# Kernel optimization log

Hardware: AMD Instinct MI355X
Metric: run time of the kernel (lower is better)

Reference implementation:

```python
import jax, jax.numpy as jnp
import numpy as np

B, NI, NH = 1024, 32, 1024  # batch, num_inputs, num_hidden


def _masks(ni, nh):
    # get_mask semantics from the torch source (mask shape = (out_features, in_features))
    in_deg_input = jnp.arange(ni) % ni                # mask_type='input'
    hid_deg = jnp.arange(nh) % (ni - 1)               # hidden degrees
    out_deg_output = jnp.arange(2 * ni) % ni - 1      # mask_type='output'
    m1 = (hid_deg[:, None] >= in_deg_input[None, :]).astype(jnp.float32)   # (NH, NI)
    m2 = (hid_deg[:, None] >= hid_deg[None, :]).astype(jnp.float32)        # (NH, NH)
    m3 = (out_deg_output[:, None] >= hid_deg[None, :]).astype(jnp.float32) # (2*NI, NH)
    return m1, m2, m3


def setup_inputs() -> dict:
    key = jax.random.key(0)
    ks = jax.random.split(key, 7)
    s1 = 1.0 / np.sqrt(NI)
    s2 = 1.0 / np.sqrt(NH)
    return {
        "inputs": jax.random.normal(ks[0], (B, NI), dtype=jnp.float32),
        "W1": jax.random.normal(ks[1], (NH, NI), dtype=jnp.float32) * s1,
        "b1": jax.random.normal(ks[2], (NH,), dtype=jnp.float32) * s1,
        "W2": jax.random.normal(ks[3], (NH, NH), dtype=jnp.float32) * s2,
        "b2": jax.random.normal(ks[4], (NH,), dtype=jnp.float32) * s2,
        "W3": jax.random.normal(ks[5], (2 * NI, NH), dtype=jnp.float32) * s2,
        "b3": jax.random.normal(ks[6], (2 * NI,), dtype=jnp.float32) * s2,
    }


def reference(inputs, W1, b1, W2, b2, W3, b3):
    ni = inputs.shape[1]
    nh = W1.shape[0]
    m1, m2, m3 = _masks(ni, nh)
    M1, M2, M3 = W1 * m1, W2 * m2, W3 * m3  # masked weights, precomputed once

    def net(x):  # 3-layer masked MLP -> (B, 2*ni) params
        h = jax.nn.relu(x @ M1.T + b1)
        h = jax.nn.relu(h @ M2.T + b2)
        return h @ M3.T + b3

    def step(x, i):
        p = net(x)                       # (B, 2*ni)
        m_i = p[:, i]                    # mean for dim i
        a_i = jnp.tanh(p[:, ni + i])     # log-scale for dim i (use_tanh=True)
        x_i = inputs[:, i] * jnp.exp(a_i) + m_i
        return x.at[:, i].set(x_i), -a_i

    x, neg_a = jax.lax.scan(step, jnp.zeros_like(inputs), jnp.arange(ni))
    J = neg_a.sum(axis=0)[:, None]       # (B, 1)
    return x, J
```

## Files before the change

kernel.cpp:

```cpp
#include <hip/hip_runtime.h>
#include <hip/hip_fp16.h>
#include <math.h>

#define NI   32
#define NH   1024
#define NB   1024

#define OFF_B1S 0
#define OFF_B2S 1056
#define OFF_W3S 2080
#define OFF_W1B 67616
#define OFF_PB  84512

__device__ __forceinline__ int base_of(int d) { return (d == 0) ? 0 : 33 * d + 1; }

__device__ __forceinline__ unsigned short f2h(float f) {
    return __half_as_ushort(__float2half(f));
}

typedef _Float16 h2v __attribute__((ext_vector_type(2)));
__device__ __forceinline__ h2v as_h2(unsigned u) {
    union { unsigned u; h2v h; } c; c.u = u; return c.h;
}
__device__ __forceinline__ float fdot2u(unsigned a, unsigned b, float c) {
#if __has_builtin(__builtin_amdgcn_fdot2)
    return __builtin_amdgcn_fdot2(as_h2(a), as_h2(b), c, false);
#else
    h2v ah = as_h2(a), bh = as_h2(b);
    return fmaf((float)ah.x, (float)bh.x, fmaf((float)ah.y, (float)bh.y, c));
#endif
}

template <int CTRL>
__device__ __forceinline__ float dpp_add(float s) {
    int t = __builtin_amdgcn_update_dpp(0, __float_as_int(s), CTRL, 0xF, 0xF, true);
    return s + __int_as_float(t);
}

__device__ __forceinline__ float wave_allsum(float s) {
    s = dpp_add<0xB1>(s);
    s = dpp_add<0x4E>(s);
    s = dpp_add<0x141>(s);
    s = dpp_add<0x140>(s);
#if __has_builtin(__builtin_amdgcn_permlane16_swap)
    {
        using uint2v = __attribute__((ext_vector_type(2))) unsigned int;
        uint2v r = __builtin_amdgcn_permlane16_swap(
            __float_as_uint(s), __float_as_uint(s), false, false);
        s = __uint_as_float(r.x) + __uint_as_float(r.y);
    }
#else
    s += __int_as_float(__builtin_amdgcn_ds_swizzle(__float_as_int(s), 0x401F));
#endif
#if __has_builtin(__builtin_amdgcn_permlane32_swap)
    {
        using uint2v = __attribute__((ext_vector_type(2))) unsigned int;
        uint2v r = __builtin_amdgcn_permlane32_swap(
            __float_as_uint(s), __float_as_uint(s), false, false);
        s = __uint_as_float(r.x) + __uint_as_float(r.y);
    }
#else
    s += __shfl_xor(s, 32, 64);
#endif
    return s;
}

template <int CNT>
__device__ __forceinline__ void prep_w2_cls(int d, int oh0, const float* __restrict__ W2,
                                            unsigned short* __restrict__ pb16, int t,
                                            float (*tile)[65]) {
    const int bse = base_of(d);
#pragma unroll 1
    for (int e = t; e < CNT * 64; e += 256) {
        int k = e >> 6, c = e & 63;
        int og = d + 31 * k;
        tile[k][c] = W2[(size_t)og * NH + oh0 + c];
    }
    __syncthreads();
#pragma unroll 1
    for (int e = t; e < 64 * CNT; e += 256) {
        int oh_l = e / CNT;
        int k = e - oh_l * CNT;
        int oh = oh0 + oh_l;
        int dd = oh % 31, u = oh / 31;
        int sg = bse + k;
        float v = (d >= dd) ? tile[k][oh_l] : 0.0f;
        size_t a = (size_t)((dd * 17 + (u >> 1)) * 256 + (sg >> 2)) * 8
                 + (sg & 3) * 2 + (u & 1);
        pb16[a] = f2h(v);
    }
}

__global__ __launch_bounds__(256) void prep_all(const float* __restrict__ W1,
        const float* __restrict__ b1, const float* __restrict__ W2,
        const float* __restrict__ b2, const float* __restrict__ W3,
        float* __restrict__ ws) {
    __shared__ float tile[34][65];
    const int bid = blockIdx.x, t = threadIdx.x;
    unsigned short* pb16 = (unsigned short*)(ws + OFF_PB);
    if (bid < 496) {
        int d = bid >> 4, oh0 = (bid & 15) * 64;
        if (d == 0) prep_w2_cls<34>(0, oh0, W2, pb16, t, tile);
        else        prep_w2_cls<33>(d, oh0, W2, pb16, t, tile);
    } else if (bid < 560) {
        const int o  = bid - 496;
        const int od = (o & 31) - 1;
#pragma unroll 1
        for (int e = t; e < NH; e += 256) {
            int dd = e % 31;
            int k  = e / 31;
            int su = (dd == 0) ? k : 33 * dd + 1 + k;
            float v = (od >= dd) ? W3[(size_t)o * NH + e] : 0.0f;
            ws[OFF_W3S + (size_t)o * NH + su] = v;
        }
    } else {
        const int og = (bid - 560) * 256 + t;
        const int dd = og % 31;
        const int k  = og / 31;
        const int su = (dd == 0) ? k : 33 * dd + 1 + k;
        ws[OFF_B1S + su] = b1[og];
        ws[OFF_B2S + su] = b2[og];
        unsigned* w1b32 = (unsigned*)(ws + OFF_W1B);
        const float4* wrow = (const float4*)(W1 + (size_t)og * NI);
        float4 r[8];
#pragma unroll
        for (int q4 = 0; q4 < 8; ++q4) r[q4] = wrow[q4];
        const float* rf = (const float*)&r[0];
#pragma unroll
        for (int jp = 0; jp < 16; ++jp) {
            float v0 = (dd >= 2 * jp)     ? rf[2 * jp]     : 0.0f;
            float v1 = (dd >= 2 * jp + 1) ? rf[2 * jp + 1] : 0.0f;
            unsigned pk = (unsigned)f2h(v0) | ((unsigned)f2h(v1) << 16);
            w1b32[(size_t)jp * 1056 + su] = pk;
        }
    }
}

__device__ __forceinline__ void consume_pair(uint4 g, uint2 av,
                                             float4& acc0, float4& acc1) {
    acc0.x = fdot2u(av.x, g.x, acc0.x);
    acc0.y = fdot2u(av.x, g.y, acc0.y);
    acc0.z = fdot2u(av.x, g.z, acc0.z);
    acc0.w = fdot2u(av.x, g.w, acc0.w);
    acc1.x = fdot2u(av.y, g.x, acc1.x);
    acc1.y = fdot2u(av.y, g.y, acc1.y);
    acc1.z = fdot2u(av.y, g.z, acc1.z);
    acc1.w = fdot2u(av.y, g.w, acc1.w);
}

__global__ __launch_bounds__(256, 2) void made_scan(
        const float* __restrict__ inputs,
        const float* __restrict__ b3,
        const float* __restrict__ ws,
        float* __restrict__ out) {
    __shared__ float    xsS[4][2][36];
    __shared__ unsigned xsH[4][2][20];
    __shared__ unsigned a1H[4][36];
    __shared__ float part[2][4][4];
    __shared__ float b3S[64];
    __shared__ float xinS[2][NI];

    const int lane = threadIdx.x & 63;
    const int w    = threadIdx.x >> 6;
    const int pairity = ((blockIdx.x >> 8) ^ blockIdx.x) & 1;
    const int q    = w ^ (pairity * 3);
    const int gb   = q * 256;
    const int row0 = blockIdx.x * 2;

    const float* b1s = ws + OFF_B1S;
    const float* b2s = ws + OFF_B2S;
    const float* W3s = ws + OFF_W3S;
    const unsigned* W1B = (const unsigned*)(ws + OFF_W1B);
    const uint4*    PB  = (const uint4*)(ws + OFF_PB);

    float4 acc0 = ((const float4*)(b2s + gb))[lane];
    float4 acc1 = acc0;
    float J0 = 0.f, J1 = 0.f;

    if (w == 0) {
        b3S[lane] = b3[lane];
        if (lane < NI) {
            xinS[0][lane] = inputs[row0 * NI + lane];
            xinS[1][lane] = inputs[(row0 + 1) * NI + lane];
        }
    }
    {
        float* px = &xsS[w][0][0];
        for (int k = lane; k < 72; k += 64) px[k] = 0.f;
        unsigned* ph = &xsH[w][0][0];
        for (int k = lane; k < 40; k += 64) ph[k] = 0u;
    }
    __syncthreads();

    {
        float p00 = b3S[0], p01 = b3S[NI];
        float e20 = __expf(2.f * fminf(p01, 15.f));
        float ta  = (e20 - 1.f) / (e20 + 1.f);
        float es  = __expf(ta);
        float x0  = fmaf(xinS[0][0], es, p00);
        float x1  = fmaf(xinS[1][0], es, p00);
        J0 -= ta; J1 -= ta;
        if (lane == 0) {
            xsS[w][0][0] = x0; xsS[w][1][0] = x1;
            ((unsigned short*)&xsH[w][0][0])[0] = f2h(x0);
            ((unsigned short*)&xsH[w][1][0])[0] = f2h(x1);
        }
    }

#pragma unroll 1
    for (int i = 1; i < NI; ++i) {
        const int dd   = i - 1;
        const int goff = base_of(dd);
        const int cnt  = (i == 1) ? 34 : 33;
        const bool doB = (gb + 256 > goff);
        const bool doC = (gb < 33 * i + 1);

        float4 wa = make_float4(0, 0, 0, 0), wb = make_float4(0, 0, 0, 0);
        if (doC) {
            wa = ((const float4*)(W3s + (size_t)i * NH + gb))[lane];
            wb = ((const float4*)(W3s + (size_t)(NI + i) * NH + gb))[lane];
        }

        if (doB) {
            const uint4* pbase = PB + (size_t)(dd * 17) * 256 + (gb >> 2) + lane;
            uint4 G1[9];
#pragma unroll
            for (int u2 = 0; u2 < 9; ++u2) G1[u2] = pbase[u2 * 256];
            __builtin_amdgcn_sched_barrier(0);

            const int su = goff + lane;
            float bz = b1s[su];
            unsigned wk[16];
#pragma unroll
            for (int k = 0; k < 16; ++k) wk[k] = W1B[k * 1056 + su];
            float zA0 = bz, zA1 = 0, zA2 = 0, zA3 = 0;
            float zB0 = bz, zB1 = 0, zB2 = 0, zB3 = 0;
#pragma unroll
            for (int q4 = 0; q4 < 4; ++q4) {
                uint4 xp0 = *(const uint4*)&xsH[w][0][4 * q4];
                uint4 xp1 = *(const uint4*)&xsH[w][1][4 * q4];
                zA0 = fdot2u(xp0.x, wk[4 * q4 + 0], zA0);
                zB0 = fdot2u(xp1.x, wk[4 * q4 + 0], zB0);
                zA1 = fdot2u(xp0.y, wk[4 * q4 + 1], zA1);
                zB1 = fdot2u(xp1.y, wk[4 * q4 + 1], zB1);
                zA2 = fdot2u(xp0.z, wk[4 * q4 + 2], zA2);
                zB2 = fdot2u(xp1.z, wk[4 * q4 + 2], zB2);
                zA3 = fdot2u(xp0.w, wk[4 * q4 + 3], zA3);
                zB3 = fdot2u(xp1.w, wk[4 * q4 + 3], zB3);
            }
            const bool ok = lane < cnt;
            float a0 = ok ? fmaxf((zA0 + zA1) + (zA2 + zA3), 0.f) : 0.f;
            float a1 = ok ? fmaxf((zB0 + zB1) + (zB2 + zB3), 0.f) : 0.f;
            if (lane < 36) {
                unsigned short* ah = (unsigned short*)&a1H[w][0];
                int u2 = lane >> 1, h = lane & 1;
                ah[u2 * 4 + h]     = f2h(a0);
                ah[u2 * 4 + 2 + h] = f2h(a1);
            }
            __builtin_amdgcn_sched_barrier(0);

            uint4 G2[8];
#pragma unroll
            for (int u2 = 0; u2 < 8; ++u2) G2[u2] = pbase[(9 + u2) * 256];
            __builtin_amdgcn_sched_barrier(0);
#pragma unroll
            for (int u2 = 0; u2 < 9; ++u2)
                consume_pair(G1[u2], *(const uint2*)&a1H[w][2 * u2], acc0, acc1);
            __builtin_amdgcn_sched_barrier(0);
#pragma unroll
            for (int u2 = 0; u2 < 8; ++u2)
                consume_pair(G2[u2], *(const uint2*)&a1H[w][18 + 2 * u2], acc0, acc1);
        }

        float s00 = 0, s01 = 0, s10 = 0, s11 = 0;
        if (doC) {
            float hx, hy, hz, hw;
            hx = fmaxf(acc0.x, 0.f); hy = fmaxf(acc0.y, 0.f);
            hz = fmaxf(acc0.z, 0.f); hw = fmaxf(acc0.w, 0.f);
            s00 = fmaf(wa.x, hx, fmaf(wa.y, hy, fmaf(wa.z, hz, wa.w * hw)));
            s01 = fmaf(wb.x, hx, fmaf(wb.y, hy, fmaf(wb.z, hz, wb.w * hw)));
            hx = fmaxf(acc1.x, 0.f); hy = fmaxf(acc1.y, 0.f);
            hz = fmaxf(acc1.z, 0.f); hw = fmaxf(acc1.w, 0.f);
            s10 = fmaf(wa.x, hx, fmaf(wa.y, hy, fmaf(wa.z, hz, wa.w * hw)));
            s11 = fmaf(wb.x, hx, fmaf(wb.y, hy, fmaf(wb.z, hz, wb.w * hw)));
            s00 = wave_allsum(s00); s01 = wave_allsum(s01);
            s10 = wave_allsum(s10); s11 = wave_allsum(s11);
        }
        if (lane == 0)
            *((float4*)&part[i & 1][w][0]) = make_float4(s00, s01, s10, s11);
        __syncthreads();

        const float* pb = &part[i & 1][0][0];
        float4 q0 = ((const float4*)pb)[0], q1 = ((const float4*)pb)[1];
        float4 q2 = ((const float4*)pb)[2], q3 = ((const float4*)pb)[3];
        float bi  = b3S[i];
        float bia = b3S[NI + i];
        float p00 = ((q0.x + q1.x) + (q2.x + q3.x)) + bi;
        float p01 = ((q0.y + q1.y) + (q2.y + q3.y)) + bia;
        float p10 = ((q0.z + q1.z) + (q2.z + q3.z)) + bi;
        float p11 = ((q0.w + q1.w) + (q2.w + q3.w)) + bia;
        float e20 = __expf(2.f * fminf(p01, 15.f));
        float ta0 = (e20 - 1.f) / (e20 + 1.f);
        float x0  = fmaf(xinS[0][i], __expf(ta0), p00);
        float e21 = __expf(2.f * fminf(p11, 15.f));
        float ta1 = (e21 - 1.f) / (e21 + 1.f);
        float x1  = fmaf(xinS[1][i], __expf(ta1), p10);
        J0 -= ta0; J1 -= ta1;
        if (lane == 0) {
            xsS[w][0][i] = x0; xsS[w][1][i] = x1;
            ((unsigned short*)&xsH[w][0][0])[i] = f2h(x0);
            ((unsigned short*)&xsH[w][1][0])[i] = f2h(x1);
        }
    }

    if (w == 0) {
        if (lane < NI) {
            out[row0 * NI + lane]       = xsS[0][0][lane];
            out[(row0 + 1) * NI + lane] = xsS[0][1][lane];
        }
        if (lane == 0) {
            out[NB * NI + row0]     = J0;
            out[NB * NI + row0 + 1] = J1;
        }
    }
}

extern "C" void kernel_launch(void* const* d_in, const int* in_sizes, int n_in,
                              void* d_out, int out_size, void* d_ws, size_t ws_size,
                              hipStream_t stream) {
    const float* inputs = (const float*)d_in[0];
    const float* W1     = (const float*)d_in[1];
    const float* b1     = (const float*)d_in[2];
    const float* W2     = (const float*)d_in[3];
    const float* b2     = (const float*)d_in[4];
    const float* W3     = (const float*)d_in[5];
    const float* b3     = (const float*)d_in[6];
    float* out = (float*)d_out;
    float* ws  = (float*)d_ws;

    prep_all<<<564, 256, 0, stream>>>(W1, b1, W2, b2, W3, ws);
    made_scan<<<NB / 2, 256, 0, stream>>>(inputs, b3, ws, out);
}
```

Before: 140.4 us.

## Prefetch next step's layer-2 weights across barrier and skip zero W1 groups

Hoists the first nine packed W2 tile loads out of the loop and prefetches the next iteration's G1 slice during the current step. The global-memory latency then overlaps the barrier and the serial tail math. The layer-1 dot product now only processes input groups that can be nonzero for step i, skipping masked W1 reads. The __syncthreads is replaced by an LDS-only waitcnt plus s_barrier, so outstanding global prefetches are not drained at the barrier. This raises register pressure from holding G1 across iterations.

```diff
diff --git a/kernel.cpp b/kernel.cpp
--- a/kernel.cpp
+++ b/kernel.cpp
@@ -207,6 +207,14 @@
         }
     }
 
+    uint4 G1[9];
+    {
+        const uint4* pb0 = PB + (gb >> 2) + lane;
+#pragma unroll
+        for (int u2 = 0; u2 < 9; ++u2) G1[u2] = pb0[u2 * 256];
+    }
+    __builtin_amdgcn_sched_barrier(0);
+
 #pragma unroll 1
     for (int i = 1; i < NI; ++i) {
         const int dd   = i - 1;
@@ -222,32 +230,27 @@
         }
 
         if (doB) {
-            const uint4* pbase = PB + (size_t)(dd * 17) * 256 + (gb >> 2) + lane;
-            uint4 G1[9];
-#pragma unroll
-            for (int u2 = 0; u2 < 9; ++u2) G1[u2] = pbase[u2 * 256];
-            __builtin_amdgcn_sched_barrier(0);
-
             const int su = goff + lane;
             float bz = b1s[su];
-            unsigned wk[16];
-#pragma unroll
-            for (int k = 0; k < 16; ++k) wk[k] = W1B[k * 1056 + su];
+            const int kmax2 = (i + 1) >> 1;
             float zA0 = bz, zA1 = 0, zA2 = 0, zA3 = 0;
             float zB0 = bz, zB1 = 0, zB2 = 0, zB3 = 0;
-#pragma unroll
-            for (int q4 = 0; q4 < 4; ++q4) {
+            auto pa_group = [&](int q4) {
                 uint4 xp0 = *(const uint4*)&xsH[w][0][4 * q4];
                 uint4 xp1 = *(const uint4*)&xsH[w][1][4 * q4];
-                zA0 = fdot2u(xp0.x, wk[4 * q4 + 0], zA0);
-                zB0 = fdot2u(xp1.x, wk[4 * q4 + 0], zB0);
-                zA1 = fdot2u(xp0.y, wk[4 * q4 + 1], zA1);
-                zB1 = fdot2u(xp1.y, wk[4 * q4 + 1], zB1);
-                zA2 = fdot2u(xp0.z, wk[4 * q4 + 2], zA2);
-                zB2 = fdot2u(xp1.z, wk[4 * q4 + 2], zB2);
-                zA3 = fdot2u(xp0.w, wk[4 * q4 + 3], zA3);
-                zB3 = fdot2u(xp1.w, wk[4 * q4 + 3], zB3);
-            }
+                unsigned wk0 = W1B[(4 * q4 + 0) * 1056 + su];
+                unsigned wk1 = W1B[(4 * q4 + 1) * 1056 + su];
+                unsigned wk2 = W1B[(4 * q4 + 2) * 1056 + su];
+                unsigned wk3 = W1B[(4 * q4 + 3) * 1056 + su];
+                zA0 = fdot2u(xp0.x, wk0, zA0); zB0 = fdot2u(xp1.x, wk0, zB0);
+                zA1 = fdot2u(xp0.y, wk1, zA1); zB1 = fdot2u(xp1.y, wk1, zB1);
+                zA2 = fdot2u(xp0.z, wk2, zA2); zB2 = fdot2u(xp1.z, wk2, zB2);
+                zA3 = fdot2u(xp0.w, wk3, zA3); zB3 = fdot2u(xp1.w, wk3, zB3);
+            };
+            pa_group(0);
+            if (kmax2 > 4)  pa_group(1);
+            if (kmax2 > 8)  pa_group(2);
+            if (kmax2 > 12) pa_group(3);
             const bool ok = lane < cnt;
             float a0 = ok ? fmaxf((zA0 + zA1) + (zA2 + zA3), 0.f) : 0.f;
             float a1 = ok ? fmaxf((zB0 + zB1) + (zB2 + zB3), 0.f) : 0.f;
@@ -261,11 +264,20 @@
 
             uint4 G2[8];
 #pragma unroll
-            for (int u2 = 0; u2 < 8; ++u2) G2[u2] = pbase[(9 + u2) * 256];
+            for (int u2 = 0; u2 < 8; ++u2) {
+                const uint4* pbase = PB + (size_t)(dd * 17) * 256 + (gb >> 2) + lane;
+                G2[u2] = pbase[(9 + u2) * 256];
+            }
             __builtin_amdgcn_sched_barrier(0);
 #pragma unroll
             for (int u2 = 0; u2 < 9; ++u2)
                 consume_pair(G1[u2], *(const uint2*)&a1H[w][2 * u2], acc0, acc1);
+
+            if (gb + 256 > 33 * i + 1) {
+                const uint4* pbn = PB + (size_t)(i * 17) * 256 + (gb >> 2) + lane;
+#pragma unroll
+                for (int u2 = 0; u2 < 9; ++u2) G1[u2] = pbn[u2 * 256];
+            }
             __builtin_amdgcn_sched_barrier(0);
 #pragma unroll
             for (int u2 = 0; u2 < 8; ++u2)
@@ -288,7 +300,11 @@
         }
         if (lane == 0)
             *((float4*)&part[i & 1][w][0]) = make_float4(s00, s01, s10, s11);
-        __syncthreads();
+
+        __builtin_amdgcn_sched_barrier(0);
+        asm volatile("s_waitcnt lgkmcnt(0)" ::: "memory");
+        __builtin_amdgcn_s_barrier();
+        __builtin_amdgcn_sched_barrier(0);
 
         const float* pb = &part[i & 1][0][0];
         float4 q0 = ((const float4*)pb)[0], q1 = ((const float4*)pb)[1];
```

Result: slower. 151.4 us (+7.8%).

## Process four batch rows per block to reuse streamed W2 weights

Applied to the files above, without the earlier changes.

Each block now handles four batch rows instead of two. Every W2/W1/W3 weight fragment loaded from global memory is reused across four rows' accumulators, which halves weight traffic per row. The grid shrinks from 512 to 256 blocks and launch bounds drop to one block per SM. The per-block parity swizzle of wave-to-column assignment is removed. The cost is more registers per thread, and the grid may be too small to fill all CUs on MI355X (256 CUs), which reduces parallelism and latency hiding.

```diff
diff --git a/kernel.cpp b/kernel.cpp
--- a/kernel.cpp
+++ b/kernel.cpp
@@ -136,36 +136,34 @@
     }
 }
 
-__device__ __forceinline__ void consume_pair(uint4 g, uint2 av,
-                                             float4& acc0, float4& acc1) {
-    acc0.x = fdot2u(av.x, g.x, acc0.x);
-    acc0.y = fdot2u(av.x, g.y, acc0.y);
-    acc0.z = fdot2u(av.x, g.z, acc0.z);
-    acc0.w = fdot2u(av.x, g.w, acc0.w);
-    acc1.x = fdot2u(av.y, g.x, acc1.x);
-    acc1.y = fdot2u(av.y, g.y, acc1.y);
-    acc1.z = fdot2u(av.y, g.z, acc1.z);
-    acc1.w = fdot2u(av.y, g.w, acc1.w);
-}
-
-__global__ __launch_bounds__(256, 2) void made_scan(
+__device__ __forceinline__ void consume_pair4(uint4 g, uint4 av,
+        float4& c0, float4& c1, float4& c2, float4& c3) {
+    c0.x = fdot2u(av.x, g.x, c0.x); c0.y = fdot2u(av.x, g.y, c0.y);
+    c0.z = fdot2u(av.x, g.z, c0.z); c0.w = fdot2u(av.x, g.w, c0.w);
+    c1.x = fdot2u(av.y, g.x, c1.x); c1.y = fdot2u(av.y, g.y, c1.y);
+    c1.z = fdot2u(av.y, g.z, c1.z); c1.w = fdot2u(av.y, g.w, c1.w);
+    c2.x = fdot2u(av.z, g.x, c2.x); c2.y = fdot2u(av.z, g.y, c2.y);
+    c2.z = fdot2u(av.z, g.z, c2.z); c2.w = fdot2u(av.z, g.w, c2.w);
+    c3.x = fdot2u(av.w, g.x, c3.x); c3.y = fdot2u(av.w, g.y, c3.y);
+    c3.z = fdot2u(av.w, g.z, c3.z); c3.w = fdot2u(av.w, g.w, c3.w);
+}
+
+__global__ __launch_bounds__(256, 1) void made_scan(
         const float* __restrict__ inputs,
         const float* __restrict__ b3,
         const float* __restrict__ ws,
         float* __restrict__ out) {
-    __shared__ float    xsS[4][2][36];
-    __shared__ unsigned xsH[4][2][20];
-    __shared__ unsigned a1H[4][36];
-    __shared__ float part[2][4][4];
-    __shared__ float b3S[64];
-    __shared__ float xinS[2][NI];
+    __shared__ float    xsS[4][4][36];
+    __shared__ unsigned xsH[4][4][20];
+    __shared__ uint4    a1H4[4][18];
+    __shared__ float    part[2][4][8];
+    __shared__ float    b3S[64];
+    __shared__ float    xinS[4][NI];
 
     const int lane = threadIdx.x & 63;
     const int w    = threadIdx.x >> 6;
-    const int pairity = ((blockIdx.x >> 8) ^ blockIdx.x) & 1;
-    const int q    = w ^ (pairity * 3);
-    const int gb   = q * 256;
-    const int row0 = blockIdx.x * 2;
+    const int gb   = w * 256;
+    const int row0 = blockIdx.x * 4;
 
     const float* b1s = ws + OFF_B1S;
     const float* b2s = ws + OFF_B2S;
@@ -173,22 +171,23 @@
     const unsigned* W1B = (const unsigned*)(ws + OFF_W1B);
     const uint4*    PB  = (const uint4*)(ws + OFF_PB);
 
-    float4 acc0 = ((const float4*)(b2s + gb))[lane];
-    float4 acc1 = acc0;
-    float J0 = 0.f, J1 = 0.f;
+    float4 bcc = ((const float4*)(b2s + gb))[lane];
+    float4 acc0 = bcc, acc1 = bcc, acc2 = bcc, acc3 = bcc;
+    float J0 = 0.f, J1 = 0.f, J2 = 0.f, J3 = 0.f;
 
     if (w == 0) {
         b3S[lane] = b3[lane];
         if (lane < NI) {
-            xinS[0][lane] = inputs[row0 * NI + lane];
-            xinS[1][lane] = inputs[(row0 + 1) * NI + lane];
+#pragma unroll
+            for (int r = 0; r < 4; ++r)
+                xinS[r][lane] = inputs[(row0 + r) * NI + lane];
         }
     }
     {
         float* px = &xsS[w][0][0];
-        for (int k = lane; k < 72; k += 64) px[k] = 0.f;
+        for (int k = lane; k < 144; k += 64) px[k] = 0.f;
         unsigned* ph = &xsH[w][0][0];
-        for (int k = lane; k < 40; k += 64) ph[k] = 0u;
+        for (int k = lane; k < 80; k += 64) ph[k] = 0u;
     }
     __syncthreads();
 
@@ -197,13 +196,18 @@
         float e20 = __expf(2.f * fminf(p01, 15.f));
         float ta  = (e20 - 1.f) / (e20 + 1.f);
         float es  = __expf(ta);
-        float x0  = fmaf(xinS[0][0], es, p00);
-        float x1  = fmaf(xinS[1][0], es, p00);
-        J0 -= ta; J1 -= ta;
+        float x0 = fmaf(xinS[0][0], es, p00);
+        float x1 = fmaf(xinS[1][0], es, p00);
+        float x2 = fmaf(xinS[2][0], es, p00);
+        float x3 = fmaf(xinS[3][0], es, p00);
+        J0 -= ta; J1 -= ta; J2 -= ta; J3 -= ta;
         if (lane == 0) {
             xsS[w][0][0] = x0; xsS[w][1][0] = x1;
+            xsS[w][2][0] = x2; xsS[w][3][0] = x3;
             ((unsigned short*)&xsH[w][0][0])[0] = f2h(x0);
             ((unsigned short*)&xsH[w][1][0])[0] = f2h(x1);
+            ((unsigned short*)&xsH[w][2][0])[0] = f2h(x2);
+            ((unsigned short*)&xsH[w][3][0])[0] = f2h(x3);
         }
     }
 
@@ -233,94 +237,138 @@
             unsigned wk[16];
 #pragma unroll
             for (int k = 0; k < 16; ++k) wk[k] = W1B[k * 1056 + su];
-            float zA0 = bz, zA1 = 0, zA2 = 0, zA3 = 0;
-            float zB0 = bz, zB1 = 0, zB2 = 0, zB3 = 0;
+            float z[4][4];
+#pragma unroll
+            for (int r = 0; r < 4; ++r) {
+                z[r][0] = bz; z[r][1] = 0.f; z[r][2] = 0.f; z[r][3] = 0.f;
+            }
 #pragma unroll
             for (int q4 = 0; q4 < 4; ++q4) {
                 uint4 xp0 = *(const uint4*)&xsH[w][0][4 * q4];
                 uint4 xp1 = *(const uint4*)&xsH[w][1][4 * q4];
-                zA0 = fdot2u(xp0.x, wk[4 * q4 + 0], zA0);
-                zB0 = fdot2u(xp1.x, wk[4 * q4 + 0], zB0);
-                zA1 = fdot2u(xp0.y, wk[4 * q4 + 1], zA1);
-                zB1 = fdot2u(xp1.y, wk[4 * q4 + 1], zB1);
-                zA2 = fdot2u(xp0.z, wk[4 * q4 + 2], zA2);
-                zB2 = fdot2u(xp1.z, wk[4 * q4 + 2], zB2);
-                zA3 = fdot2u(xp0.w, wk[4 * q4 + 3], zA3);
-                zB3 = fdot2u(xp1.w, wk[4 * q4 + 3], zB3);
+                uint4 xp2 = *(const uint4*)&xsH[w][2][4 * q4];
+                uint4 xp3 = *(const uint4*)&xsH[w][3][4 * q4];
+                unsigned k0 = wk[4 * q4 + 0], k1 = wk[4 * q4 + 1];
+                unsigned k2 = wk[4 * q4 + 2], k3 = wk[4 * q4 + 3];
+                z[0][0] = fdot2u(xp0.x, k0, z[0][0]);
+                z[0][1] = fdot2u(xp0.y, k1, z[0][1]);
+                z[0][2] = fdot2u(xp0.z, k2, z[0][2]);
+                z[0][3] = fdot2u(xp0.w, k3, z[0][3]);
+                z[1][0] = fdot2u(xp1.x, k0, z[1][0]);
+                z[1][1] = fdot2u(xp1.y, k1, z[1][1]);
+                z[1][2] = fdot2u(xp1.z, k2, z[1][2]);
+                z[1][3] = fdot2u(xp1.w, k3, z[1][3]);
+                z[2][0] = fdot2u(xp2.x, k0, z[2][0]);
+                z[2][1] = fdot2u(xp2.y, k1, z[2][1]);
+                z[2][2] = fdot2u(xp2.z, k2, z[2][2]);
+                z[2][3] = fdot2u(xp2.w, k3, z[2][3]);
+                z[3][0] = fdot2u(xp3.x, k0, z[3][0]);
+                z[3][1] = fdot2u(xp3.y, k1, z[3][1]);
+                z[3][2] = fdot2u(xp3.z, k2, z[3][2]);
+                z[3][3] = fdot2u(xp3.w, k3, z[3][3]);
             }
             const bool ok = lane < cnt;
-            float a0 = ok ? fmaxf((zA0 + zA1) + (zA2 + zA3), 0.f) : 0.f;
-            float a1 = ok ? fmaxf((zB0 + zB1) + (zB2 + zB3), 0.f) : 0.f;
+            float a0 = ok ? fmaxf((z[0][0] + z[0][1]) + (z[0][2] + z[0][3]), 0.f) : 0.f;
+            float a1 = ok ? fmaxf((z[1][0] + z[1][1]) + (z[1][2] + z[1][3]), 0.f) : 0.f;
+            float a2 = ok ? fmaxf((z[2][0] + z[2][1]) + (z[2][2] + z[2][3]), 0.f) : 0.f;
+            float a3 = ok ? fmaxf((z[3][0] + z[3][1]) + (z[3][2] + z[3][3]), 0.f) : 0.f;
             if (lane < 36) {
-                unsigned short* ah = (unsigned short*)&a1H[w][0];
+                unsigned short* ah = (unsigned short*)&a1H4[w][0];
                 int u2 = lane >> 1, h = lane & 1;
-                ah[u2 * 4 + h]     = f2h(a0);
-                ah[u2 * 4 + 2 + h] = f2h(a1);
+                ah[u2 * 8 + 0 + h] = f2h(a0);
+                ah[u2 * 8 + 2 + h] = f2h(a1);
+                ah[u2 * 8 + 4 + h] = f2h(a2);
+                ah[u2 * 8 + 6 + h] = f2h(a3);
             }
             __builtin_amdgcn_sched_barrier(0);
 
             uint4 G2[8];
-#pragma unroll
-            for (int u2 = 0; u2 < 8; ++u2) G2[u2] = pbase[(9 + u2) * 256];
+            {
+#pragma unroll
+                for (int u2 = 0; u2 < 8; ++u2) G2[u2] = pbase[(9 + u2) * 256];
+            }
             __builtin_amdgcn_sched_barrier(0);
 #pragma unroll
             for (int u2 = 0; u2 < 9; ++u2)
-                consume_pair(G1[u2], *(const uint2*)&a1H[w][2 * u2], acc0, acc1);
+                consume_pair4(G1[u2], a1H4[w][u2], acc0, acc1, acc2, acc3);
             __builtin_amdgcn_sched_barrier(0);
 #pragma unroll
             for (int u2 = 0; u2 < 8; ++u2)
-                consume_pair(G2[u2], *(const uint2*)&a1H[w][18 + 2 * u2], acc0, acc1);
-        }
-
-        float s00 = 0, s01 = 0, s10 = 0, s11 = 0;
+                consume_pair4(G2[u2], a1H4[w][9 + u2], acc0, acc1, acc2, acc3);
+        }
+
+        float s0[4] = {0, 0, 0, 0}, s1[4] = {0, 0, 0, 0};
         if (doC) {
             float hx, hy, hz, hw;
-            hx = fmaxf(acc0.x, 0.f); hy = fmaxf(acc0.y, 0.f);
-            hz = fmaxf(acc0.z, 0.f); hw = fmaxf(acc0.w, 0.f);
-            s00 = fmaf(wa.x, hx, fmaf(wa.y, hy, fmaf(wa.z, hz, wa.w * hw)));
-            s01 = fmaf(wb.x, hx, fmaf(wb.y, hy, fmaf(wb.z, hz, wb.w * hw)));
-            hx = fmaxf(acc1.x, 0.f); hy = fmaxf(acc1.y, 0.f);
-            hz = fmaxf(acc1.z, 0.f); hw = fmaxf(acc1.w, 0.f);
-            s10 = fmaf(wa.x, hx, fmaf(wa.y, hy, fmaf(wa.z, hz, wa.w * hw)));
-            s11 = fmaf(wb.x, hx, fmaf(wb.y, hy, fmaf(wb.z, hz, wb.w * hw)));
-            s00 = wave_allsum(s00); s01 = wave_allsum(s01);
-            s10 = wave_allsum(s10); s11 = wave_allsum(s11);
-        }
-        if (lane == 0)
-            *((float4*)&part[i & 1][w][0]) = make_float4(s00, s01, s10, s11);
+#define PHASEC_ROW(r, ACC)                                                  \
+            hx = fmaxf(ACC.x, 0.f); hy = fmaxf(ACC.y, 0.f);                 \
+            hz = fmaxf(ACC.z, 0.f); hw = fmaxf(ACC.w, 0.f);                 \
+            s0[r] = fmaf(wa.x, hx, fmaf(wa.y, hy, fmaf(wa.z, hz, wa.w * hw))); \
+            s1[r] = fmaf(wb.x, hx, fmaf(wb.y, hy, fmaf(wb.z, hz, wb.w * hw)));
+            PHASEC_ROW(0, acc0)
+            PHASEC_ROW(1, acc1)
+            PHASEC_ROW(2, acc2)
+            PHASEC_ROW(3, acc3)
+#undef PHASEC_ROW
+#pragma unroll
+            for (int r = 0; r < 4; ++r) {
+                s0[r] = wave_allsum(s0[r]);
+                s1[r] = wave_allsum(s1[r]);
+            }
+        }
+        if (lane == 0) {
+            *((float4*)&part[i & 1][w][0]) = make_float4(s0[0], s0[1], s0[2], s0[3]);
+            *((float4*)&part[i & 1][w][4]) = make_float4(s1[0], s1[1], s1[2], s1[3]);
+        }
         __syncthreads();
 
         const float* pb = &part[i & 1][0][0];
-        float4 q0 = ((const float4*)pb)[0], q1 = ((const float4*)pb)[1];
-        float4 q2 = ((const float4*)pb)[2], q3 = ((const float4*)pb)[3];
+        float4 A0 = ((const float4*)pb)[0], B0 = ((const float4*)pb)[1];
+        float4 A1 = ((const float4*)pb)[2], B1 = ((const float4*)pb)[3];
+        float4 A2 = ((const float4*)pb)[4], B2 = ((const float4*)pb)[5];
+        float4 A3 = ((const float4*)pb)[6], B3 = ((const float4*)pb)[7];
         float bi  = b3S[i];
         float bia = b3S[NI + i];
-        float p00 = ((q0.x + q1.x) + (q2.x + q3.x)) + bi;
-        float p01 = ((q0.y + q1.y) + (q2.y + q3.y)) + bia;
-        float p10 = ((q0.z + q1.z) + (q2.z + q3.z)) + bi;
-        float p11 = ((q0.w + q1.w) + (q2.w + q3.w)) + bia;
-        float e20 = __expf(2.f * fminf(p01, 15.f));
-        float ta0 = (e20 - 1.f) / (e20 + 1.f);
-        float x0  = fmaf(xinS[0][i], __expf(ta0), p00);
-        float e21 = __expf(2.f * fminf(p11, 15.f));
-        float ta1 = (e21 - 1.f) / (e21 + 1.f);
-        float x1  = fmaf(xinS[1][i], __expf(ta1), p10);
-        J0 -= ta0; J1 -= ta1;
+        float p0[4], p1[4];
+        p0[0] = ((A0.x + A1.x) + (A2.x + A3.x)) + bi;
+        p0[1] = ((A0.y + A1.y) + (A2.y + A3.y)) + bi;
+        p0[2] = ((A0.z + A1.z) + (A2.z + A3.z)) + bi;
+        p0[3] = ((A0.w + A1.w) + (A2.w + A3.w)) + bi;
+        p1[0] = ((B0.x + B1.x) + (B2.x + B3.x)) + bia;
+        p1[1] = ((B0.y + B1.y) + (B2.y + B3.y)) + bia;
+        p1[2] = ((B0.z + B1.z) + (B2.z + B3.z)) + bia;
+        p1[3] = ((B0.w + B1.w) + (B2.w + B3.w)) + bia;
+        float xr[4];
+#pragma unroll
+        for (int r = 0; r < 4; ++r) {
+            float e2 = __expf(2.f * fminf(p1[r], 15.f));
+            float ta = (e2 - 1.f) / (e2 + 1.f);
+            xr[r] = fmaf(xinS[r][i], __expf(ta), p0[r]);
+            if (r == 0) J0 -= ta;
+            if (r == 1) J1 -= ta;
+            if (r == 2) J2 -= ta;
+            if (r == 3) J3 -= ta;
+        }
         if (lane == 0) {
-            xsS[w][0][i] = x0; xsS[w][1][i] = x1;
-            ((unsigned short*)&xsH[w][0][0])[i] = f2h(x0);
-            ((unsigned short*)&xsH[w][1][0])[i] = f2h(x1);
+#pragma unroll
+            for (int r = 0; r < 4; ++r) {
+                xsS[w][r][i] = xr[r];
+                ((unsigned short*)&xsH[w][r][0])[i] = f2h(xr[r]);
+            }
         }
     }
 
     if (w == 0) {
         if (lane < NI) {
-            out[row0 * NI + lane]       = xsS[0][0][lane];
-            out[(row0 + 1) * NI + lane] = xsS[0][1][lane];
+#pragma unroll
+            for (int r = 0; r < 4; ++r)
+                out[(row0 + r) * NI + lane] = xsS[0][r][lane];
         }
         if (lane == 0) {
-            out[NB * NI + row0]     = J0;
+            out[NB * NI + row0 + 0] = J0;
             out[NB * NI + row0 + 1] = J1;
+            out[NB * NI + row0 + 2] = J2;
+            out[NB * NI + row0 + 3] = J3;
         }
     }
 }
@@ -339,5 +387,5 @@
     float* ws  = (float*)d_ws;
 
     prep_all<<<564, 256, 0, stream>>>(W1, b1, W2, b2, W3, ws);
-    made_scan<<<NB / 2, 256, 0, stream>>>(inputs, b3, ws, out);
-}
+    made_scan<<<NB / 4, 256, 0, stream>>>(inputs, b3, ws, out);
+}
```

New measurement: 153.9 us. 9.6% more time.

## Fuse weight prep and scan into one cooperative kernel with grid sync

Applied to the files above, without the earlier changes.

Merges the weight-preparation kernel and the autoregressive scan kernel into a single cooperative launch. Each block first does its share of the prep work (blocks below 52 take an extra unit) and loads its per-block inputs, then all blocks meet at a grid-wide barrier before the scan runs. This removes one kernel launch and the gap between the two kernels. In exchange it adds a grid sync, puts 34x65 floats of tile storage in shared memory for the whole kernel (which may reduce occupancy), and requires all 512 blocks to be resident at once.

```diff
diff --git a/kernel.cpp b/kernel.cpp
--- a/kernel.cpp
+++ b/kernel.cpp
@@ -1,6 +1,9 @@
 #include <hip/hip_runtime.h>
 #include <hip/hip_fp16.h>
+#include <hip/hip_cooperative_groups.h>
 #include <math.h>
+
+namespace cg = cooperative_groups;
 
 #define NI   32
 #define NH   1024
@@ -91,19 +94,18 @@
     }
 }
 
-__global__ __launch_bounds__(256) void prep_all(const float* __restrict__ W1,
-        const float* __restrict__ b1, const float* __restrict__ W2,
-        const float* __restrict__ b2, const float* __restrict__ W3,
-        float* __restrict__ ws) {
-    __shared__ float tile[34][65];
-    const int bid = blockIdx.x, t = threadIdx.x;
+__device__ __forceinline__ void prep_unit(int u, int t,
+        const float* __restrict__ W1, const float* __restrict__ b1,
+        const float* __restrict__ W2, const float* __restrict__ b2,
+        const float* __restrict__ W3, float* __restrict__ ws,
+        float (*tile)[65]) {
     unsigned short* pb16 = (unsigned short*)(ws + OFF_PB);
-    if (bid < 496) {
-        int d = bid >> 4, oh0 = (bid & 15) * 64;
+    if (u < 496) {
+        int d = u >> 4, oh0 = (u & 15) * 64;
         if (d == 0) prep_w2_cls<34>(0, oh0, W2, pb16, t, tile);
         else        prep_w2_cls<33>(d, oh0, W2, pb16, t, tile);
-    } else if (bid < 560) {
-        const int o  = bid - 496;
+    } else if (u < 560) {
+        const int o  = u - 496;
         const int od = (o & 31) - 1;
 #pragma unroll 1
         for (int e = t; e < NH; e += 256) {
@@ -114,7 +116,7 @@
             ws[OFF_W3S + (size_t)o * NH + su] = v;
         }
     } else {
-        const int og = (bid - 560) * 256 + t;
+        const int og = (u - 560) * 256 + t;
         const int dd = og % 31;
         const int k  = og / 31;
         const int su = (dd == 0) ? k : 33 * dd + 1 + k;
@@ -148,11 +150,13 @@
     acc1.w = fdot2u(av.y, g.w, acc1.w);
 }
 
-__global__ __launch_bounds__(256, 2) void made_scan(
+__global__ __launch_bounds__(256, 2) void fused_made(
         const float* __restrict__ inputs,
-        const float* __restrict__ b3,
-        const float* __restrict__ ws,
-        float* __restrict__ out) {
+        const float* __restrict__ W1, const float* __restrict__ b1,
+        const float* __restrict__ W2, const float* __restrict__ b2,
+        const float* __restrict__ W3, const float* __restrict__ b3,
+        float* __restrict__ ws, float* __restrict__ out) {
+    __shared__ float tile[34][65];
     __shared__ float    xsS[4][2][36];
     __shared__ unsigned xsH[4][2][20];
     __shared__ unsigned a1H[4][36];
@@ -160,12 +164,33 @@
     __shared__ float b3S[64];
     __shared__ float xinS[2][NI];
 
-    const int lane = threadIdx.x & 63;
-    const int w    = threadIdx.x >> 6;
-    const int pairity = ((blockIdx.x >> 8) ^ blockIdx.x) & 1;
+    const int bid  = blockIdx.x;
+    const int t    = threadIdx.x;
+    const int lane = t & 63;
+    const int w    = t >> 6;
+    const int pairity = ((bid >> 8) ^ bid) & 1;
     const int q    = w ^ (pairity * 3);
     const int gb   = q * 256;
-    const int row0 = blockIdx.x * 2;
+    const int row0 = bid * 2;
+
+    prep_unit(bid, t, W1, b1, W2, b2, W3, ws, tile);
+    if (bid < 52) prep_unit(512 + bid, t, W1, b1, W2, b2, W3, ws, tile);
+
+    if (w == 0) {
+        b3S[lane] = b3[lane];
+        if (lane < NI) {
+            xinS[0][lane] = inputs[row0 * NI + lane];
+            xinS[1][lane] = inputs[(row0 + 1) * NI + lane];
+        }
+    }
+    {
+        float* px = &xsS[w][0][0];
+        for (int k = lane; k < 72; k += 64) px[k] = 0.f;
+        unsigned* ph = &xsH[w][0][0];
+        for (int k = lane; k < 40; k += 64) ph[k] = 0u;
+    }
+
+    cg::this_grid().sync();
 
     const float* b1s = ws + OFF_B1S;
     const float* b2s = ws + OFF_B2S;
@@ -176,21 +201,6 @@
     float4 acc0 = ((const float4*)(b2s + gb))[lane];
     float4 acc1 = acc0;
     float J0 = 0.f, J1 = 0.f;
-
-    if (w == 0) {
-        b3S[lane] = b3[lane];
-        if (lane < NI) {
-            xinS[0][lane] = inputs[row0 * NI + lane];
-            xinS[1][lane] = inputs[(row0 + 1) * NI + lane];
-        }
-    }
-    {
-        float* px = &xsS[w][0][0];
-        for (int k = lane; k < 72; k += 64) px[k] = 0.f;
-        unsigned* ph = &xsH[w][0][0];
-        for (int k = lane; k < 40; k += 64) ph[k] = 0u;
-    }
-    __syncthreads();
 
     {
         float p00 = b3S[0], p01 = b3S[NI];
@@ -338,6 +348,8 @@
     float* out = (float*)d_out;
     float* ws  = (float*)d_ws;
 
-    prep_all<<<564, 256, 0, stream>>>(W1, b1, W2, b2, W3, ws);
-    made_scan<<<NB / 2, 256, 0, stream>>>(inputs, b3, ws, out);
-}
+    void* args[] = {(void*)&inputs, (void*)&W1, (void*)&b1, (void*)&W2,
+                    (void*)&b2, (void*)&W3, (void*)&b3, (void*)&ws, (void*)&out};
+    hipLaunchCooperativeKernel((const void*)fused_made, dim3(NB / 2), dim3(256),
+                               args, 0, stream);
+}
```

New measurement: 213.2 us. 1.52x slower.
